# Kernel optimization log

Hardware: AMD Instinct MI355X
Metric: run time of the kernel (lower is better)

The kernel has to match this reference:

```python
import jax, jax.numpy as jnp
import numpy as np

B, H, S, D = 2, 16, 2048, 64

def setup_inputs() -> dict:
    key = jax.random.key(0)
    kq, kk, kv, km = jax.random.split(key, 4)
    Q = jax.random.normal(kq, (B, H, S, D), dtype=jnp.float32)
    K = jax.random.normal(kk, (B, H, S, D), dtype=jnp.float32)
    V = jax.random.normal(kv, (B, H, S, D), dtype=jnp.float32)
    # padding-style boolean mask, broadcast over heads; True = masked out
    attn_mask = jax.random.randint(km, (B, 1, S, S), 0, 2).astype(jnp.bool_)
    return {"Q": Q, "K": K, "V": V, "attn_mask": attn_mask}

def reference(Q, K, V, attn_mask):
    d = Q.shape[-1]
    scale = 1.0 / np.sqrt(d).astype(np.float32)
    # [B,H,S,S] scores
    scores = jnp.einsum('bhqd,bhkd->bhqk', Q, K) * scale
    scores = jnp.where(attn_mask, jnp.float32(-1e9), scores)
    attn = jax.nn.softmax(scores, axis=-1)
    context = jnp.einsum('bhqk,bhkd->bhqd', attn, V)
    return context
```

## Files before the change

### kernel.cpp

```cpp
#include <hip/hip_runtime.h>

#define B_ 2
#define H_ 16
#define S_ 2048
#define D_ 64
#define BK 32
#define NKT (S_ / BK)
#define QSCALE 0.18033688011112042f
#define MFIX 16.0f

#define KSD 36
#define VTD 18
#define KS_SZ (BK * KSD)
#define VT_SZ (D_ * VTD)

typedef __attribute__((ext_vector_type(4))) float  float4v;
typedef __attribute__((ext_vector_type(2))) _Float16 half2v;
typedef __attribute__((ext_vector_type(4))) _Float16 half4v;
typedef __attribute__((ext_vector_type(8))) _Float16 half8v;
typedef __attribute__((ext_vector_type(2))) __fp16 fp16x2;
typedef __attribute__((ext_vector_type(2))) unsigned uint2v;

union H2U { half2v h; fp16x2 g; unsigned u; };
union H4U { half4v h4; half2v h2[2]; fp16x2 g2[2]; uint2v u2; };
union H8U { half8v h8; fp16x2 g2[4]; };

__device__ __forceinline__ unsigned pkh(float a, float b) {
    H2U c; c.g = __builtin_amdgcn_cvt_pkrtz(a, b);
    return c.u;
}
__device__ __forceinline__ float fexp2(float x) {
#if __has_builtin(__builtin_amdgcn_exp2f)
    return __builtin_amdgcn_exp2f(x);
#else
    return exp2f(x);
#endif
}

__device__ __forceinline__ void wg_barrier() {
    asm volatile("s_waitcnt lgkmcnt(0)\n\ts_barrier" ::: "memory");
}

struct Stage { float4 k0, k1, va, vb; };

__device__ __forceinline__ void stage_load(const float* __restrict__ Kg,
                                           const float* __restrict__ Vg,
                                           int kk, int dd, Stage& s) {
    s.k0 = *(const float4*)(Kg + (size_t)kk * D_ + dd);
    s.k1 = *(const float4*)(Kg + (size_t)(kk + 16) * D_ + dd);
    s.va = *(const float4*)(Vg + (size_t)(2 * kk) * D_ + dd);
    s.vb = *(const float4*)(Vg + (size_t)(2 * kk + 1) * D_ + dd);
}

__device__ __forceinline__ void stage_store(unsigned* KsB, unsigned* VtB,
                                            int kwa, int kwb, const int* vw,
                                            const Stage& s) {
    *(uint2v*)&KsB[kwa] = (uint2v){ pkh(s.k0.x, s.k0.y), pkh(s.k0.z, s.k0.w) };
    *(uint2v*)&KsB[kwb] = (uint2v){ pkh(s.k1.x, s.k1.y), pkh(s.k1.z, s.k1.w) };
    VtB[vw[0]] = pkh(s.va.x, s.vb.x);
    VtB[vw[1]] = pkh(s.va.y, s.vb.y);
    VtB[vw[2]] = pkh(s.va.z, s.vb.z);
    VtB[vw[3]] = pkh(s.va.w, s.vb.w);
}

__device__ __forceinline__ float4 mask2bias(int4 m) {
    float4 r;
    r.x = m.x ? -1e9f : -MFIX;  r.y = m.y ? -1e9f : -MFIX;
    r.z = m.z ? -1e9f : -MFIX;  r.w = m.w ? -1e9f : -MFIX;
    return r;
}

__global__ __launch_bounds__(256, 4)
void attn_flash_st(const float* __restrict__ Q, const float* __restrict__ K,
                   const float* __restrict__ V, const int* __restrict__ mask,
                   float* __restrict__ out)
{
    __shared__ unsigned KsAll[2 * KS_SZ];
    __shared__ unsigned VtAll[2 * VT_SZ];

    const int tid  = threadIdx.x;
    const int lane = tid & 63;
    const int l15  = lane & 15;
    const int quad = lane >> 4;
    const int wave = tid >> 6;
    const int bh   = blockIdx.y;
    const int b    = bh / H_;
    const int qbase = blockIdx.x * 64 + wave * 16;
    const size_t qkv = (size_t)bh * S_ * D_;

    half8v qf[2];
    {
        const float* qrow = Q + qkv + (size_t)(qbase + l15) * D_ + quad * 8;
        #pragma unroll
        for (int dc = 0; dc < 2; ++dc) {
            float4 f0 = *(const float4*)(qrow + dc * 32);
            float4 f1 = *(const float4*)(qrow + dc * 32 + 4);
            H8U u;
            u.g2[0] = __builtin_amdgcn_cvt_pkrtz(f0.x * QSCALE, f0.y * QSCALE);
            u.g2[1] = __builtin_amdgcn_cvt_pkrtz(f0.z * QSCALE, f0.w * QSCALE);
            u.g2[2] = __builtin_amdgcn_cvt_pkrtz(f1.x * QSCALE, f1.y * QSCALE);
            u.g2[3] = __builtin_amdgcn_cvt_pkrtz(f1.z * QSCALE, f1.w * QSCALE);
            qf[dc] = u.h8;
        }
    }

    const int kk = tid >> 4;
    const int dd = (tid & 15) * 4;
    const int kwa = kk * KSD + (tid & 15) * 2;
    const int kwb = (kk + 16) * KSD + (tid & 15) * 2;
    int vw[4];
    #pragma unroll
    for (int m = 0; m < 4; ++m)
        vw[m] = (dd + m) * VTD + (kk ^ ((((dd + m) >> 4) & 3) << 1));

    int kroff[2][2];
    #pragma unroll
    for (int t = 0; t < 2; ++t)
        #pragma unroll
        for (int dc = 0; dc < 2; ++dc)
            kroff[t][dc] = (t * 16 + l15) * KSD + dc * 16 + quad * 4;
    int vrd[4][2];
    #pragma unroll
    for (int nb = 0; nb < 4; ++nb)
        #pragma unroll
        for (int t = 0; t < 2; ++t)
            vrd[nb][t] = (nb * 16 + l15) * VTD + ((t * 8 + quad * 2) ^ ((nb & 3) << 1));

    const int* mrow0 = mask + (size_t)b * S_ * S_ + (size_t)(qbase + l15) * S_ + quad * 4;

    float l_lane = 0.0f;
    float4v o[4];
    #pragma unroll
    for (int nb = 0; nb < 4; ++nb) o[nb] = (float4v){0.f, 0.f, 0.f, 0.f};

    const float* Kg0 = K + qkv;
    const float* Vg0 = V + qkv;

    Stage sA, sB;
    stage_load(Kg0, Vg0, kk, dd, sA);
    stage_store(KsAll, VtAll, kwa, kwb, vw, sA);
    stage_load(Kg0 + BK * D_, Vg0 + BK * D_, kk, dd, sB);
    float4 mk0 = mask2bias(*(const int4*)(mrow0));
    float4 mk1 = mask2bias(*(const int4*)(mrow0 + 16));
    wg_barrier();

    auto iter = [&](int kt, const unsigned* KsB, const unsigned* VtB,
                    unsigned* KsN, unsigned* VtN, Stage& pre, Stage& sto) {
        const int ktn = (kt + 2 < NKT) ? kt + 2 : NKT - 1;
        stage_load(Kg0 + (size_t)ktn * BK * D_, Vg0 + (size_t)ktn * BK * D_, kk, dd, pre);
        const int mtn = (kt + 1 < NKT) ? kt + 1 : NKT - 1;
        const int* mnext = mrow0 + (size_t)mtn * BK;
        const float4 nm0 = mask2bias(*(const int4*)(mnext));
        const float4 nm1 = mask2bias(*(const int4*)(mnext + 16));

        float4v st0 = (float4v){0.f,0.f,0.f,0.f}, st1 = st0;
        {
            half8v kf;
            kf = *(const half8v*)&KsB[kroff[0][0]];
            st0 = __builtin_amdgcn_mfma_f32_16x16x32_f16(kf, qf[0], st0, 0, 0, 0);
            kf = *(const half8v*)&KsB[kroff[0][1]];
            st0 = __builtin_amdgcn_mfma_f32_16x16x32_f16(kf, qf[1], st0, 0, 0, 0);
            kf = *(const half8v*)&KsB[kroff[1][0]];
            st1 = __builtin_amdgcn_mfma_f32_16x16x32_f16(kf, qf[0], st1, 0, 0, 0);
            kf = *(const half8v*)&KsB[kroff[1][1]];
            st1 = __builtin_amdgcn_mfma_f32_16x16x32_f16(kf, qf[1], st1, 0, 0, 0);
        }

        float4v p0, p1;
        p0.x = fexp2(st0.x + mk0.x); p0.y = fexp2(st0.y + mk0.y);
        p0.z = fexp2(st0.z + mk0.z); p0.w = fexp2(st0.w + mk0.w);
        p1.x = fexp2(st1.x + mk1.x); p1.y = fexp2(st1.y + mk1.y);
        p1.z = fexp2(st1.z + mk1.z); p1.w = fexp2(st1.w + mk1.w);

        l_lane += ((p0.x + p0.y) + (p0.z + p0.w)) +
                  ((p1.x + p1.y) + (p1.z + p1.w));

        H4U pf0u, pf1u;
        pf0u.g2[0] = __builtin_amdgcn_cvt_pkrtz(p0.x, p0.y);
        pf0u.g2[1] = __builtin_amdgcn_cvt_pkrtz(p0.z, p0.w);
        pf1u.g2[0] = __builtin_amdgcn_cvt_pkrtz(p1.x, p1.y);
        pf1u.g2[1] = __builtin_amdgcn_cvt_pkrtz(p1.z, p1.w);

        #pragma unroll
        for (int nb = 0; nb < 4; ++nb) {
            H4U vf;
            vf.u2 = *(const uint2v*)&VtB[vrd[nb][0]];
            o[nb] = __builtin_amdgcn_mfma_f32_16x16x16f16(vf.h4, pf0u.h4, o[nb], 0, 0, 0);
            vf.u2 = *(const uint2v*)&VtB[vrd[nb][1]];
            o[nb] = __builtin_amdgcn_mfma_f32_16x16x16f16(vf.h4, pf1u.h4, o[nb], 0, 0, 0);
        }

        stage_store(KsN, VtN, kwa, kwb, vw, sto);
        wg_barrier();
        mk0 = nm0; mk1 = nm1;
    };

    #pragma unroll 1
    for (int kt2 = 0; kt2 < NKT; kt2 += 2) {
        iter(kt2,     KsAll,         VtAll,         (unsigned*)KsAll + KS_SZ, (unsigned*)VtAll + VT_SZ, sA, sB);
        iter(kt2 + 1, KsAll + KS_SZ, VtAll + VT_SZ, (unsigned*)KsAll,         (unsigned*)VtAll,         sB, sA);
    }

    float ls = l_lane;
    ls += __shfl_xor(ls, 16, 64);
    ls += __shfl_xor(ls, 32, 64);
    const float inv = 1.0f / ls;

    float* orow = out + qkv + (size_t)(qbase + l15) * D_ + quad * 4;
    #pragma unroll
    for (int nb = 0; nb < 4; ++nb) {
        float4 ov = { o[nb].x * inv, o[nb].y * inv, o[nb].z * inv, o[nb].w * inv };
        *(float4*)(orow + nb * 16) = ov;
    }
}

extern "C" void kernel_launch(void* const* d_in, const int* in_sizes, int n_in,
                              void* d_out, int out_size, void* d_ws, size_t ws_size,
                              hipStream_t stream) {
    const float* Q    = (const float*)d_in[0];
    const float* K    = (const float*)d_in[1];
    const float* V    = (const float*)d_in[2];
    const int*   mask = (const int*)d_in[3];
    float* out = (float*)d_out;

    dim3 grid(S_ / 64, B_ * H_);
    dim3 block(256);
    attn_flash_st<<<grid, block, 0, stream>>>(Q, K, V, mask, out);
}
```

Measured before the change: 196.7 us.

## Split key dimension across two blocks and combine partial outputs

Adds a split-K flash attention path: each of two z-blocks handles half the key tiles and writes unnormalized partial outputs and row sums to workspace, then a combine kernel sums and normalizes them. This doubles the grid to raise parallelism and occupancy (launch bounds raised to 8 blocks) on a grid of only 1024 blocks. It costs extra global traffic for the partials and a second kernel launch, and it falls back to the old kernel if the workspace is too small. The fixed softmax offset makes the partials directly additive without max rescaling.

```diff
diff --git a/kernel.cpp b/kernel.cpp
--- a/kernel.cpp
+++ b/kernel.cpp
@@ -6,6 +6,8 @@
 #define D_ 64
 #define BK 32
 #define NKT (S_ / BK)
+#define ZSPLIT 2
+#define NKT_Z (NKT / ZSPLIT)
 #define QSCALE 0.18033688011112042f
 #define MFIX 16.0f
 
@@ -13,6 +15,9 @@
 #define VTD 18
 #define KS_SZ (BK * KSD)
 #define VT_SZ (D_ * VTD)
+
+#define BHSD ((size_t)B_ * H_ * S_ * D_)
+#define BHS  ((size_t)B_ * H_ * S_)
 
 typedef __attribute__((ext_vector_type(4))) float  float4v;
 typedef __attribute__((ext_vector_type(2))) _Float16 half2v;
@@ -70,10 +75,10 @@
     return r;
 }
 
-__global__ __launch_bounds__(256, 4)
-void attn_flash_st(const float* __restrict__ Q, const float* __restrict__ K,
+__global__ __launch_bounds__(256, 8)
+void attn_flash_sk(const float* __restrict__ Q, const float* __restrict__ K,
                    const float* __restrict__ V, const int* __restrict__ mask,
-                   float* __restrict__ out)
+                   float* __restrict__ Opart, float* __restrict__ Lpart)
 {
     __shared__ unsigned KsAll[2 * KS_SZ];
     __shared__ unsigned VtAll[2 * VT_SZ];
@@ -88,6 +93,9 @@
     const int qbase = blockIdx.x * 64 + wave * 16;
     const size_t qkv = (size_t)bh * S_ * D_;
 
+    const int ktBegin = blockIdx.z * NKT_Z;
+    const int ktEnd   = ktBegin + NKT_Z;
+
     half8v qf[2];
     {
         const float* qrow = Q + qkv + (size_t)(qbase + l15) * D_ + quad * 8;
@@ -137,18 +145,18 @@
     const float* Vg0 = V + qkv;
 
     Stage sA, sB;
-    stage_load(Kg0, Vg0, kk, dd, sA);
+    stage_load(Kg0 + (size_t)ktBegin * BK * D_, Vg0 + (size_t)ktBegin * BK * D_, kk, dd, sA);
     stage_store(KsAll, VtAll, kwa, kwb, vw, sA);
-    stage_load(Kg0 + BK * D_, Vg0 + BK * D_, kk, dd, sB);
-    float4 mk0 = mask2bias(*(const int4*)(mrow0));
-    float4 mk1 = mask2bias(*(const int4*)(mrow0 + 16));
+    stage_load(Kg0 + (size_t)(ktBegin + 1) * BK * D_, Vg0 + (size_t)(ktBegin + 1) * BK * D_, kk, dd, sB);
+    float4 mk0 = mask2bias(*(const int4*)(mrow0 + (size_t)ktBegin * BK));
+    float4 mk1 = mask2bias(*(const int4*)(mrow0 + (size_t)ktBegin * BK + 16));
     wg_barrier();
 
     auto iter = [&](int kt, const unsigned* KsB, const unsigned* VtB,
                     unsigned* KsN, unsigned* VtN, Stage& pre, Stage& sto) {
-        const int ktn = (kt + 2 < NKT) ? kt + 2 : NKT - 1;
+        const int ktn = (kt + 2 < ktEnd) ? kt + 2 : ktEnd - 1;
         stage_load(Kg0 + (size_t)ktn * BK * D_, Vg0 + (size_t)ktn * BK * D_, kk, dd, pre);
-        const int mtn = (kt + 1 < NKT) ? kt + 1 : NKT - 1;
+        const int mtn = (kt + 1 < ktEnd) ? kt + 1 : ktEnd - 1;
         const int* mnext = mrow0 + (size_t)mtn * BK;
         const float4 nm0 = mask2bias(*(const int4*)(mnext));
         const float4 nm1 = mask2bias(*(const int4*)(mnext + 16));
@@ -196,6 +204,167 @@
     };
 
     #pragma unroll 1
+    for (int kt2 = ktBegin; kt2 < ktEnd; kt2 += 2) {
+        iter(kt2,     KsAll,         VtAll,         (unsigned*)KsAll + KS_SZ, (unsigned*)VtAll + VT_SZ, sA, sB);
+        iter(kt2 + 1, KsAll + KS_SZ, VtAll + VT_SZ, (unsigned*)KsAll,         (unsigned*)VtAll,         sB, sA);
+    }
+
+    float ls = l_lane;
+    ls += __shfl_xor(ls, 16, 64);
+    ls += __shfl_xor(ls, 32, 64);
+
+    float* orow = Opart + (size_t)blockIdx.z * BHSD + qkv
+                  + (size_t)(qbase + l15) * D_ + quad * 4;
+    #pragma unroll
+    for (int nb = 0; nb < 4; ++nb) {
+        float4 ov = { o[nb].x, o[nb].y, o[nb].z, o[nb].w };
+        *(float4*)(orow + nb * 16) = ov;
+    }
+    if (quad == 0)
+        Lpart[(size_t)blockIdx.z * BHS + (size_t)bh * S_ + qbase + l15] = ls;
+}
+
+__global__ __launch_bounds__(256)
+void attn_combine(const float* __restrict__ Opart, const float* __restrict__ Lpart,
+                  float* __restrict__ out)
+{
+    const size_t i = (size_t)blockIdx.x * 256 + threadIdx.x;
+    const size_t row = i >> 4;
+    const float l = Lpart[row] + Lpart[BHS + row];
+    const float inv = 1.0f / l;
+    const float4 a = ((const float4*)Opart)[i];
+    const float4 c = ((const float4*)Opart)[BHSD / 4 + i];
+    float4 r = { (a.x + c.x) * inv, (a.y + c.y) * inv,
+                 (a.z + c.z) * inv, (a.w + c.w) * inv };
+    ((float4*)out)[i] = r;
+}
+
+__global__ __launch_bounds__(256, 4)
+void attn_flash_st(const float* __restrict__ Q, const float* __restrict__ K,
+                   const float* __restrict__ V, const int* __restrict__ mask,
+                   float* __restrict__ out)
+{
+    __shared__ unsigned KsAll[2 * KS_SZ];
+    __shared__ unsigned VtAll[2 * VT_SZ];
+
+    const int tid  = threadIdx.x;
+    const int lane = tid & 63;
+    const int l15  = lane & 15;
+    const int quad = lane >> 4;
+    const int wave = tid >> 6;
+    const int bh   = blockIdx.y;
+    const int b    = bh / H_;
+    const int qbase = blockIdx.x * 64 + wave * 16;
+    const size_t qkv = (size_t)bh * S_ * D_;
+
+    half8v qf[2];
+    {
+        const float* qrow = Q + qkv + (size_t)(qbase + l15) * D_ + quad * 8;
+        #pragma unroll
+        for (int dc = 0; dc < 2; ++dc) {
+            float4 f0 = *(const float4*)(qrow + dc * 32);
+            float4 f1 = *(const float4*)(qrow + dc * 32 + 4);
+            H8U u;
+            u.g2[0] = __builtin_amdgcn_cvt_pkrtz(f0.x * QSCALE, f0.y * QSCALE);
+            u.g2[1] = __builtin_amdgcn_cvt_pkrtz(f0.z * QSCALE, f0.w * QSCALE);
+            u.g2[2] = __builtin_amdgcn_cvt_pkrtz(f1.x * QSCALE, f1.y * QSCALE);
+            u.g2[3] = __builtin_amdgcn_cvt_pkrtz(f1.z * QSCALE, f1.w * QSCALE);
+            qf[dc] = u.h8;
+        }
+    }
+
+    const int kk = tid >> 4;
+    const int dd = (tid & 15) * 4;
+    const int kwa = kk * KSD + (tid & 15) * 2;
+    const int kwb = (kk + 16) * KSD + (tid & 15) * 2;
+    int vw[4];
+    #pragma unroll
+    for (int m = 0; m < 4; ++m)
+        vw[m] = (dd + m) * VTD + (kk ^ ((((dd + m) >> 4) & 3) << 1));
+
+    int kroff[2][2];
+    #pragma unroll
+    for (int t = 0; t < 2; ++t)
+        #pragma unroll
+        for (int dc = 0; dc < 2; ++dc)
+            kroff[t][dc] = (t * 16 + l15) * KSD + dc * 16 + quad * 4;
+    int vrd[4][2];
+    #pragma unroll
+    for (int nb = 0; nb < 4; ++nb)
+        #pragma unroll
+        for (int t = 0; t < 2; ++t)
+            vrd[nb][t] = (nb * 16 + l15) * VTD + ((t * 8 + quad * 2) ^ ((nb & 3) << 1));
+
+    const int* mrow0 = mask + (size_t)b * S_ * S_ + (size_t)(qbase + l15) * S_ + quad * 4;
+
+    float l_lane = 0.0f;
+    float4v o[4];
+    #pragma unroll
+    for (int nb = 0; nb < 4; ++nb) o[nb] = (float4v){0.f, 0.f, 0.f, 0.f};
+
+    const float* Kg0 = K + qkv;
+    const float* Vg0 = V + qkv;
+
+    Stage sA, sB;
+    stage_load(Kg0, Vg0, kk, dd, sA);
+    stage_store(KsAll, VtAll, kwa, kwb, vw, sA);
+    stage_load(Kg0 + BK * D_, Vg0 + BK * D_, kk, dd, sB);
+    float4 mk0 = mask2bias(*(const int4*)(mrow0));
+    float4 mk1 = mask2bias(*(const int4*)(mrow0 + 16));
+    wg_barrier();
+
+    auto iter = [&](int kt, const unsigned* KsB, const unsigned* VtB,
+                    unsigned* KsN, unsigned* VtN, Stage& pre, Stage& sto) {
+        const int ktn = (kt + 2 < NKT) ? kt + 2 : NKT - 1;
+        stage_load(Kg0 + (size_t)ktn * BK * D_, Vg0 + (size_t)ktn * BK * D_, kk, dd, pre);
+        const int mtn = (kt + 1 < NKT) ? kt + 1 : NKT - 1;
+        const int* mnext = mrow0 + (size_t)mtn * BK;
+        const float4 nm0 = mask2bias(*(const int4*)(mnext));
+        const float4 nm1 = mask2bias(*(const int4*)(mnext + 16));
+
+        float4v st0 = (float4v){0.f,0.f,0.f,0.f}, st1 = st0;
+        {
+            half8v kf;
+            kf = *(const half8v*)&KsB[kroff[0][0]];
+            st0 = __builtin_amdgcn_mfma_f32_16x16x32_f16(kf, qf[0], st0, 0, 0, 0);
+            kf = *(const half8v*)&KsB[kroff[0][1]];
+            st0 = __builtin_amdgcn_mfma_f32_16x16x32_f16(kf, qf[1], st0, 0, 0, 0);
+            kf = *(const half8v*)&KsB[kroff[1][0]];
+            st1 = __builtin_amdgcn_mfma_f32_16x16x32_f16(kf, qf[0], st1, 0, 0, 0);
+            kf = *(const half8v*)&KsB[kroff[1][1]];
+            st1 = __builtin_amdgcn_mfma_f32_16x16x32_f16(kf, qf[1], st1, 0, 0, 0);
+        }
+
+        float4v p0, p1;
+        p0.x = fexp2(st0.x + mk0.x); p0.y = fexp2(st0.y + mk0.y);
+        p0.z = fexp2(st0.z + mk0.z); p0.w = fexp2(st0.w + mk0.w);
+        p1.x = fexp2(st1.x + mk1.x); p1.y = fexp2(st1.y + mk1.y);
+        p1.z = fexp2(st1.z + mk1.z); p1.w = fexp2(st1.w + mk1.w);
+
+        l_lane += ((p0.x + p0.y) + (p0.z + p0.w)) +
+                  ((p1.x + p1.y) + (p1.z + p1.w));
+
+        H4U pf0u, pf1u;
+        pf0u.g2[0] = __builtin_amdgcn_cvt_pkrtz(p0.x, p0.y);
+        pf0u.g2[1] = __builtin_amdgcn_cvt_pkrtz(p0.z, p0.w);
+        pf1u.g2[0] = __builtin_amdgcn_cvt_pkrtz(p1.x, p1.y);
+        pf1u.g2[1] = __builtin_amdgcn_cvt_pkrtz(p1.z, p1.w);
+
+        #pragma unroll
+        for (int nb = 0; nb < 4; ++nb) {
+            H4U vf;
+            vf.u2 = *(const uint2v*)&VtB[vrd[nb][0]];
+            o[nb] = __builtin_amdgcn_mfma_f32_16x16x16f16(vf.h4, pf0u.h4, o[nb], 0, 0, 0);
+            vf.u2 = *(const uint2v*)&VtB[vrd[nb][1]];
+            o[nb] = __builtin_amdgcn_mfma_f32_16x16x16f16(vf.h4, pf1u.h4, o[nb], 0, 0, 0);
+        }
+
+        stage_store(KsN, VtN, kwa, kwb, vw, sto);
+        wg_barrier();
+        mk0 = nm0; mk1 = nm1;
+    };
+
+    #pragma unroll 1
     for (int kt2 = 0; kt2 < NKT; kt2 += 2) {
         iter(kt2,     KsAll,         VtAll,         (unsigned*)KsAll + KS_SZ, (unsigned*)VtAll + VT_SZ, sA, sB);
         iter(kt2 + 1, KsAll + KS_SZ, VtAll + VT_SZ, (unsigned*)KsAll,         (unsigned*)VtAll,         sB, sA);
@@ -223,7 +392,19 @@
     const int*   mask = (const int*)d_in[3];
     float* out = (float*)d_out;
 
-    dim3 grid(S_ / 64, B_ * H_);
-    dim3 block(256);
-    attn_flash_st<<<grid, block, 0, stream>>>(Q, K, V, mask, out);
-}
+    const size_t opBytes = BHSD * ZSPLIT * sizeof(float);
+    const size_t lpBytes = BHS  * ZSPLIT * sizeof(float);
+    const size_t needFull = opBytes + lpBytes;
+
+    if (d_ws && ws_size >= needFull) {
+        float* Opart = (float*)d_ws;
+        float* Lpart = (float*)((char*)d_ws + opBytes);
+        attn_flash_sk<<<dim3(S_ / 64, B_ * H_, ZSPLIT), dim3(256), 0, stream>>>(
+            Q, K, V, mask, Opart, Lpart);
+        attn_combine<<<dim3((unsigned)(BHSD / 4 / 256)), dim3(256), 0, stream>>>(
+            Opart, Lpart, out);
+    } else {
+        attn_flash_st<<<dim3(S_ / 64, B_ * H_), dim3(256), 0, stream>>>(
+            Q, K, V, mask, out);
+    }
+}
```

Measured after the change: 601.4 us. 3.06x slower.

## Software-pipeline softmax of tile k with PV matmul of tile k-1

Applied to the files above, without the earlier changes.

Restructures the key-tile loop so each iteration issues the QK^T MFMAs for the current tile, then the PV MFMAs for the previous tile's probabilities, then computes exp/convert for the current tile. The goal is to hide the exp and convert latency behind independent MFMA work and break the serial QK→softmax→PV dependency chain. The V tile is now triple-buffered in LDS, with a prologue, a loop unrolled by six and an epilogue. This adds shared memory and register pressure and makes the buffer rotation more intricate.

```diff
diff --git a/kernel.cpp b/kernel.cpp
--- a/kernel.cpp
+++ b/kernel.cpp
@@ -71,12 +71,12 @@
 }
 
 __global__ __launch_bounds__(256, 4)
-void attn_flash_st(const float* __restrict__ Q, const float* __restrict__ K,
+void attn_flash_pl(const float* __restrict__ Q, const float* __restrict__ K,
                    const float* __restrict__ V, const int* __restrict__ mask,
                    float* __restrict__ out)
 {
-    __shared__ unsigned KsAll[2 * KS_SZ];
-    __shared__ unsigned VtAll[2 * VT_SZ];
+    __shared__ unsigned Ks[2 * KS_SZ];
+    __shared__ unsigned Vt[3 * VT_SZ];
 
     const int tid  = threadIdx.x;
     const int lane = tid & 63;
@@ -132,20 +132,56 @@
     float4v o[4];
     #pragma unroll
     for (int nb = 0; nb < 4; ++nb) o[nb] = (float4v){0.f, 0.f, 0.f, 0.f};
+    H4U pfP0, pfP1;
 
     const float* Kg0 = K + qkv;
     const float* Vg0 = V + qkv;
 
     Stage sA, sB;
     stage_load(Kg0, Vg0, kk, dd, sA);
-    stage_store(KsAll, VtAll, kwa, kwb, vw, sA);
+    stage_store(Ks, Vt, kwa, kwb, vw, sA);
     stage_load(Kg0 + BK * D_, Vg0 + BK * D_, kk, dd, sB);
     float4 mk0 = mask2bias(*(const int4*)(mrow0));
     float4 mk1 = mask2bias(*(const int4*)(mrow0 + 16));
     wg_barrier();
 
-    auto iter = [&](int kt, const unsigned* KsB, const unsigned* VtB,
-                    unsigned* KsN, unsigned* VtN, Stage& pre, Stage& sto) {
+    auto qkmm = [&](const unsigned* KsC, float4v& st0, float4v& st1) {
+        half8v kf;
+        kf = *(const half8v*)&KsC[kroff[0][0]];
+        st0 = __builtin_amdgcn_mfma_f32_16x16x32_f16(kf, qf[0], st0, 0, 0, 0);
+        kf = *(const half8v*)&KsC[kroff[0][1]];
+        st0 = __builtin_amdgcn_mfma_f32_16x16x32_f16(kf, qf[1], st0, 0, 0, 0);
+        kf = *(const half8v*)&KsC[kroff[1][0]];
+        st1 = __builtin_amdgcn_mfma_f32_16x16x32_f16(kf, qf[0], st1, 0, 0, 0);
+        kf = *(const half8v*)&KsC[kroff[1][1]];
+        st1 = __builtin_amdgcn_mfma_f32_16x16x32_f16(kf, qf[1], st1, 0, 0, 0);
+    };
+    auto softmax_cvt = [&](const float4v& st0, const float4v& st1) {
+        float4v p0, p1;
+        p0.x = fexp2(st0.x + mk0.x); p0.y = fexp2(st0.y + mk0.y);
+        p0.z = fexp2(st0.z + mk0.z); p0.w = fexp2(st0.w + mk0.w);
+        p1.x = fexp2(st1.x + mk1.x); p1.y = fexp2(st1.y + mk1.y);
+        p1.z = fexp2(st1.z + mk1.z); p1.w = fexp2(st1.w + mk1.w);
+        l_lane += ((p0.x + p0.y) + (p0.z + p0.w)) +
+                  ((p1.x + p1.y) + (p1.z + p1.w));
+        pfP0.g2[0] = __builtin_amdgcn_cvt_pkrtz(p0.x, p0.y);
+        pfP0.g2[1] = __builtin_amdgcn_cvt_pkrtz(p0.z, p0.w);
+        pfP1.g2[0] = __builtin_amdgcn_cvt_pkrtz(p1.x, p1.y);
+        pfP1.g2[1] = __builtin_amdgcn_cvt_pkrtz(p1.z, p1.w);
+    };
+    auto pvmm = [&](const unsigned* VtP) {
+        #pragma unroll
+        for (int nb = 0; nb < 4; ++nb) {
+            H4U vf;
+            vf.u2 = *(const uint2v*)&VtP[vrd[nb][0]];
+            o[nb] = __builtin_amdgcn_mfma_f32_16x16x16f16(vf.h4, pfP0.h4, o[nb], 0, 0, 0);
+            vf.u2 = *(const uint2v*)&VtP[vrd[nb][1]];
+            o[nb] = __builtin_amdgcn_mfma_f32_16x16x16f16(vf.h4, pfP1.h4, o[nb], 0, 0, 0);
+        }
+    };
+
+    auto iterD = [&](int kt, const unsigned* KsC, const unsigned* VtP,
+                     unsigned* KsN, unsigned* VtN, Stage& pre, Stage& sto) {
         const int ktn = (kt + 2 < NKT) ? kt + 2 : NKT - 1;
         stage_load(Kg0 + (size_t)ktn * BK * D_, Vg0 + (size_t)ktn * BK * D_, kk, dd, pre);
         const int mtn = (kt + 1 < NKT) ? kt + 1 : NKT - 1;
@@ -154,52 +190,41 @@
         const float4 nm1 = mask2bias(*(const int4*)(mnext + 16));
 
         float4v st0 = (float4v){0.f,0.f,0.f,0.f}, st1 = st0;
-        {
-            half8v kf;
-            kf = *(const half8v*)&KsB[kroff[0][0]];
-            st0 = __builtin_amdgcn_mfma_f32_16x16x32_f16(kf, qf[0], st0, 0, 0, 0);
-            kf = *(const half8v*)&KsB[kroff[0][1]];
-            st0 = __builtin_amdgcn_mfma_f32_16x16x32_f16(kf, qf[1], st0, 0, 0, 0);
-            kf = *(const half8v*)&KsB[kroff[1][0]];
-            st1 = __builtin_amdgcn_mfma_f32_16x16x32_f16(kf, qf[0], st1, 0, 0, 0);
-            kf = *(const half8v*)&KsB[kroff[1][1]];
-            st1 = __builtin_amdgcn_mfma_f32_16x16x32_f16(kf, qf[1], st1, 0, 0, 0);
-        }
-
-        float4v p0, p1;
-        p0.x = fexp2(st0.x + mk0.x); p0.y = fexp2(st0.y + mk0.y);
-        p0.z = fexp2(st0.z + mk0.z); p0.w = fexp2(st0.w + mk0.w);
-        p1.x = fexp2(st1.x + mk1.x); p1.y = fexp2(st1.y + mk1.y);
-        p1.z = fexp2(st1.z + mk1.z); p1.w = fexp2(st1.w + mk1.w);
-
-        l_lane += ((p0.x + p0.y) + (p0.z + p0.w)) +
-                  ((p1.x + p1.y) + (p1.z + p1.w));
-
-        H4U pf0u, pf1u;
-        pf0u.g2[0] = __builtin_amdgcn_cvt_pkrtz(p0.x, p0.y);
-        pf0u.g2[1] = __builtin_amdgcn_cvt_pkrtz(p0.z, p0.w);
-        pf1u.g2[0] = __builtin_amdgcn_cvt_pkrtz(p1.x, p1.y);
-        pf1u.g2[1] = __builtin_amdgcn_cvt_pkrtz(p1.z, p1.w);
-
-        #pragma unroll
-        for (int nb = 0; nb < 4; ++nb) {
-            H4U vf;
-            vf.u2 = *(const uint2v*)&VtB[vrd[nb][0]];
-            o[nb] = __builtin_amdgcn_mfma_f32_16x16x16f16(vf.h4, pf0u.h4, o[nb], 0, 0, 0);
-            vf.u2 = *(const uint2v*)&VtB[vrd[nb][1]];
-            o[nb] = __builtin_amdgcn_mfma_f32_16x16x16f16(vf.h4, pf1u.h4, o[nb], 0, 0, 0);
-        }
-
+        qkmm(KsC, st0, st1);
+        pvmm(VtP);
         stage_store(KsN, VtN, kwa, kwb, vw, sto);
+        softmax_cvt(st0, st1);
         wg_barrier();
         mk0 = nm0; mk1 = nm1;
     };
 
+    {
+        stage_load(Kg0 + 2 * BK * D_, Vg0 + 2 * BK * D_, kk, dd, sA);
+        const int* mnext = mrow0 + BK;
+        const float4 nm0 = mask2bias(*(const int4*)(mnext));
+        const float4 nm1 = mask2bias(*(const int4*)(mnext + 16));
+        float4v st0 = (float4v){0.f,0.f,0.f,0.f}, st1 = st0;
+        qkmm(Ks, st0, st1);
+        stage_store(Ks + KS_SZ, Vt + VT_SZ, kwa, kwb, vw, sB);
+        softmax_cvt(st0, st1);
+        wg_barrier();
+        mk0 = nm0; mk1 = nm1;
+    }
+
     #pragma unroll 1
-    for (int kt2 = 0; kt2 < NKT; kt2 += 2) {
-        iter(kt2,     KsAll,         VtAll,         (unsigned*)KsAll + KS_SZ, (unsigned*)VtAll + VT_SZ, sA, sB);
-        iter(kt2 + 1, KsAll + KS_SZ, VtAll + VT_SZ, (unsigned*)KsAll,         (unsigned*)VtAll,         sB, sA);
-    }
+    for (int t = 0; t < 10; ++t) {
+        const int k = 1 + 6 * t;
+        iterD(k,     Ks + KS_SZ, Vt,             Ks,         Vt + 2*VT_SZ, sB, sA);
+        iterD(k + 1, Ks,         Vt + VT_SZ,     Ks + KS_SZ, Vt,           sA, sB);
+        iterD(k + 2, Ks + KS_SZ, Vt + 2*VT_SZ,   Ks,         Vt + VT_SZ,   sB, sA);
+        iterD(k + 3, Ks,         Vt,             Ks + KS_SZ, Vt + 2*VT_SZ, sA, sB);
+        iterD(k + 4, Ks + KS_SZ, Vt + VT_SZ,     Ks,         Vt,           sB, sA);
+        iterD(k + 5, Ks,         Vt + 2*VT_SZ,   Ks + KS_SZ, Vt + VT_SZ,   sA, sB);
+    }
+    iterD(61, Ks + KS_SZ, Vt,             Ks,         Vt + 2*VT_SZ, sB, sA);
+    iterD(62, Ks,         Vt + VT_SZ,     Ks + KS_SZ, Vt,           sA, sB);
+    iterD(63, Ks + KS_SZ, Vt + 2*VT_SZ,   Ks,         Vt + VT_SZ,   sB, sA);
+    pvmm(Vt);
 
     float ls = l_lane;
     ls += __shfl_xor(ls, 16, 64);
@@ -223,7 +248,6 @@
     const int*   mask = (const int*)d_in[3];
     float* out = (float*)d_out;
 
-    dim3 grid(S_ / 64, B_ * H_);
-    dim3 block(256);
-    attn_flash_st<<<grid, block, 0, stream>>>(Q, K, V, mask, out);
-}
+    attn_flash_pl<<<dim3(S_ / 64, B_ * H_), dim3(256), 0, stream>>>(
+        Q, K, V, mask, out);
+}
```

New measurement: 215.7 us. 1.1x slower.

## Pre-pack K/V into MFMA fragment layout and split KV across blocks

Applied to the files above, without the earlier changes.

Adds a pre-pass kernel that converts K and V to fp16 and stores them in a global image already arranged in per-lane MFMA fragment order. The main kernel then loads fragments straight from global memory with no LDS staging or barriers, and splits the KV range in two (split-K) with an XCD-aware block mapping. A combine kernel adds the two partial outputs and divides by the summed denominators. This removes LDS traffic and synchronisation and doubles the block count, at the cost of two extra launches, fp32 partial buffers in workspace, and an extra pass over the output. The old kernel remains as a fallback when the workspace is too small.

```diff
diff --git a/kernel.cpp b/kernel.cpp
--- a/kernel.cpp
+++ b/kernel.cpp
@@ -9,10 +9,13 @@
 #define QSCALE 0.18033688011112042f
 #define MFIX 16.0f
 
-#define KSD 36
-#define VTD 18
-#define KS_SZ (BK * KSD)
-#define VT_SZ (D_ * VTD)
+#define KFRAG_OFF(t, dc) (((t) * 2 + (dc)) * 256)
+#define VFRAG_OFF(nb, t) (1024 + ((nb) * 2 + (t)) * 128)
+#define TILE2_DW 2048
+
+#define BHSD ((size_t)B_ * H_ * S_ * D_)
+#define BHS  ((size_t)B_ * H_ * S_)
+#define IMG2_DW ((size_t)B_ * H_ * NKT * TILE2_DW)
 
 typedef __attribute__((ext_vector_type(4))) float  float4v;
 typedef __attribute__((ext_vector_type(2))) _Float16 half2v;
@@ -20,10 +23,11 @@
 typedef __attribute__((ext_vector_type(8))) _Float16 half8v;
 typedef __attribute__((ext_vector_type(2))) __fp16 fp16x2;
 typedef __attribute__((ext_vector_type(2))) unsigned uint2v;
+typedef __attribute__((ext_vector_type(4))) unsigned uint4v;
 
 union H2U { half2v h; fp16x2 g; unsigned u; };
 union H4U { half4v h4; half2v h2[2]; fp16x2 g2[2]; uint2v u2; };
-union H8U { half8v h8; fp16x2 g2[4]; };
+union H8U { half8v h8; fp16x2 g2[4]; uint4v u4; };
 
 __device__ __forceinline__ unsigned pkh(float a, float b) {
     H2U c; c.g = __builtin_amdgcn_cvt_pkrtz(a, b);
@@ -39,6 +43,192 @@
 
 __device__ __forceinline__ void wg_barrier() {
     asm volatile("s_waitcnt lgkmcnt(0)\n\ts_barrier" ::: "memory");
+}
+
+__global__ __launch_bounds__(256)
+void pack_kv2(const float* __restrict__ K, const float* __restrict__ V,
+              unsigned* __restrict__ img)
+{
+    __shared__ float Kf[32 * 64];
+    __shared__ float Vf[32 * 64];
+    const int tid = threadIdx.x;
+    const int kt = blockIdx.x, bh = blockIdx.y;
+    const size_t base = ((size_t)bh * S_ + (size_t)kt * 32) * D_;
+
+    const int rr = tid >> 4, c4 = (tid & 15) * 4;
+    *(float4*)&Kf[rr * 64 + c4]        = *(const float4*)(K + base + (size_t)rr * D_ + c4);
+    *(float4*)&Kf[(rr + 16) * 64 + c4] = *(const float4*)(K + base + (size_t)(rr + 16) * D_ + c4);
+    *(float4*)&Vf[rr * 64 + c4]        = *(const float4*)(V + base + (size_t)rr * D_ + c4);
+    *(float4*)&Vf[(rr + 16) * 64 + c4] = *(const float4*)(V + base + (size_t)(rr + 16) * D_ + c4);
+    __syncthreads();
+
+    unsigned* out = img + (size_t)(bh * NKT + kt) * TILE2_DW;
+    const int lane = tid & 63, wave = tid >> 6;
+    const int l15 = lane & 15, quad = lane >> 4;
+
+    if (wave < 2) {
+        const int t = wave;
+        const int row = t * 16 + l15;
+        #pragma unroll
+        for (int dc = 0; dc < 2; ++dc) {
+            const int d0 = dc * 32 + quad * 8;
+            const float* kr = &Kf[row * 64 + d0];
+            uint4v v = { pkh(kr[0], kr[1]), pkh(kr[2], kr[3]),
+                         pkh(kr[4], kr[5]), pkh(kr[6], kr[7]) };
+            *(uint4v*)&out[KFRAG_OFF(t, dc) + lane * 4] = v;
+        }
+    } else {
+        const int nbb = (wave - 2) * 2;
+        #pragma unroll
+        for (int nbo = 0; nbo < 2; ++nbo) {
+            const int nb = nbb + nbo;
+            const int d = nb * 16 + l15;
+            #pragma unroll
+            for (int t = 0; t < 2; ++t) {
+                const int k0 = t * 16 + quad * 4;
+                uint2v v = { pkh(Vf[k0 * 64 + d],       Vf[(k0 + 1) * 64 + d]),
+                             pkh(Vf[(k0 + 2) * 64 + d], Vf[(k0 + 3) * 64 + d]) };
+                *(uint2v*)&out[VFRAG_OFF(nb, t) + lane * 2] = v;
+            }
+        }
+    }
+}
+
+__global__ __launch_bounds__(256, 4)
+void attn_frag(const float* __restrict__ Q, const unsigned* __restrict__ img,
+               const int* __restrict__ mask,
+               float* __restrict__ Opart, float* __restrict__ Lpart)
+{
+    const int tid  = threadIdx.x;
+    const int lane = tid & 63;
+    const int l15  = lane & 15;
+    const int quad = lane >> 4;
+    const int wave = tid >> 6;
+
+    const int id    = blockIdx.x;
+    const int xcd   = id & 7;
+    const int local = id >> 3;
+    const int bh_l  = local >> 6;
+    const int rem   = local & 63;
+    const int z     = rem >> 5;
+    const int qb    = rem & 31;
+    const int bh    = xcd * 4 + bh_l;
+    const int b     = bh / H_;
+    const int qbase = qb * 64 + wave * 16;
+    const size_t qkv = (size_t)bh * S_ * D_;
+    const int ktB = z * (NKT / 2);
+
+    half8v qf[2];
+    {
+        const float* qrow = Q + qkv + (size_t)(qbase + l15) * D_ + quad * 8;
+        #pragma unroll
+        for (int dc = 0; dc < 2; ++dc) {
+            float4 f0 = *(const float4*)(qrow + dc * 32);
+            float4 f1 = *(const float4*)(qrow + dc * 32 + 4);
+            H8U u;
+            u.g2[0] = __builtin_amdgcn_cvt_pkrtz(f0.x * QSCALE, f0.y * QSCALE);
+            u.g2[1] = __builtin_amdgcn_cvt_pkrtz(f0.z * QSCALE, f0.w * QSCALE);
+            u.g2[2] = __builtin_amdgcn_cvt_pkrtz(f1.x * QSCALE, f1.y * QSCALE);
+            u.g2[3] = __builtin_amdgcn_cvt_pkrtz(f1.z * QSCALE, f1.w * QSCALE);
+            qf[dc] = u.h8;
+        }
+    }
+
+    const unsigned* tp  = img + (size_t)(bh * NKT + ktB) * TILE2_DW;
+    const unsigned* kfb = tp + lane * 4;
+    const unsigned* vfb = tp + lane * 2;
+
+    const int* mrow = mask + (size_t)b * S_ * S_ + (size_t)(qbase + l15) * S_
+                      + quad * 4 + (size_t)ktB * BK;
+
+    float l_lane = 0.0f;
+    float4v o[4];
+    #pragma unroll
+    for (int nb = 0; nb < 4; ++nb) o[nb] = (float4v){0.f, 0.f, 0.f, 0.f};
+
+    #pragma unroll 2
+    for (int ktl = 0; ktl < NKT / 2; ++ktl) {
+        H8U k00, k01, k10, k11;
+        k00.u4 = *(const uint4v*)(kfb + KFRAG_OFF(0, 0));
+        k01.u4 = *(const uint4v*)(kfb + KFRAG_OFF(0, 1));
+        k10.u4 = *(const uint4v*)(kfb + KFRAG_OFF(1, 0));
+        k11.u4 = *(const uint4v*)(kfb + KFRAG_OFF(1, 1));
+        H4U v00, v01, v10, v11, v20, v21, v30, v31;
+        v00.u2 = *(const uint2v*)(vfb + VFRAG_OFF(0, 0));
+        v01.u2 = *(const uint2v*)(vfb + VFRAG_OFF(0, 1));
+        v10.u2 = *(const uint2v*)(vfb + VFRAG_OFF(1, 0));
+        v11.u2 = *(const uint2v*)(vfb + VFRAG_OFF(1, 1));
+        v20.u2 = *(const uint2v*)(vfb + VFRAG_OFF(2, 0));
+        v21.u2 = *(const uint2v*)(vfb + VFRAG_OFF(2, 1));
+        v30.u2 = *(const uint2v*)(vfb + VFRAG_OFF(3, 0));
+        v31.u2 = *(const uint2v*)(vfb + VFRAG_OFF(3, 1));
+        const int4 m0 = *(const int4*)(mrow);
+        const int4 m1 = *(const int4*)(mrow + 16);
+        kfb += TILE2_DW; vfb += TILE2_DW; mrow += BK;
+
+        float4v st0 = (float4v){0.f, 0.f, 0.f, 0.f}, st1 = st0;
+        st0 = __builtin_amdgcn_mfma_f32_16x16x32_f16(k00.h8, qf[0], st0, 0, 0, 0);
+        st0 = __builtin_amdgcn_mfma_f32_16x16x32_f16(k01.h8, qf[1], st0, 0, 0, 0);
+        st1 = __builtin_amdgcn_mfma_f32_16x16x32_f16(k10.h8, qf[0], st1, 0, 0, 0);
+        st1 = __builtin_amdgcn_mfma_f32_16x16x32_f16(k11.h8, qf[1], st1, 0, 0, 0);
+
+        float4v p0, p1;
+        p0.x = fexp2(st0.x + (m0.x ? -1e9f : -MFIX));
+        p0.y = fexp2(st0.y + (m0.y ? -1e9f : -MFIX));
+        p0.z = fexp2(st0.z + (m0.z ? -1e9f : -MFIX));
+        p0.w = fexp2(st0.w + (m0.w ? -1e9f : -MFIX));
+        p1.x = fexp2(st1.x + (m1.x ? -1e9f : -MFIX));
+        p1.y = fexp2(st1.y + (m1.y ? -1e9f : -MFIX));
+        p1.z = fexp2(st1.z + (m1.z ? -1e9f : -MFIX));
+        p1.w = fexp2(st1.w + (m1.w ? -1e9f : -MFIX));
+
+        l_lane += ((p0.x + p0.y) + (p0.z + p0.w)) +
+                  ((p1.x + p1.y) + (p1.z + p1.w));
+
+        H4U pf0, pf1;
+        pf0.g2[0] = __builtin_amdgcn_cvt_pkrtz(p0.x, p0.y);
+        pf0.g2[1] = __builtin_amdgcn_cvt_pkrtz(p0.z, p0.w);
+        pf1.g2[0] = __builtin_amdgcn_cvt_pkrtz(p1.x, p1.y);
+        pf1.g2[1] = __builtin_amdgcn_cvt_pkrtz(p1.z, p1.w);
+
+        o[0] = __builtin_amdgcn_mfma_f32_16x16x16f16(v00.h4, pf0.h4, o[0], 0, 0, 0);
+        o[0] = __builtin_amdgcn_mfma_f32_16x16x16f16(v01.h4, pf1.h4, o[0], 0, 0, 0);
+        o[1] = __builtin_amdgcn_mfma_f32_16x16x16f16(v10.h4, pf0.h4, o[1], 0, 0, 0);
+        o[1] = __builtin_amdgcn_mfma_f32_16x16x16f16(v11.h4, pf1.h4, o[1], 0, 0, 0);
+        o[2] = __builtin_amdgcn_mfma_f32_16x16x16f16(v20.h4, pf0.h4, o[2], 0, 0, 0);
+        o[2] = __builtin_amdgcn_mfma_f32_16x16x16f16(v21.h4, pf1.h4, o[2], 0, 0, 0);
+        o[3] = __builtin_amdgcn_mfma_f32_16x16x16f16(v30.h4, pf0.h4, o[3], 0, 0, 0);
+        o[3] = __builtin_amdgcn_mfma_f32_16x16x16f16(v31.h4, pf1.h4, o[3], 0, 0, 0);
+    }
+
+    float ls = l_lane;
+    ls += __shfl_xor(ls, 16, 64);
+    ls += __shfl_xor(ls, 32, 64);
+
+    float* orow = Opart + (size_t)z * BHSD + qkv
+                  + (size_t)(qbase + l15) * D_ + quad * 4;
+    #pragma unroll
+    for (int nb = 0; nb < 4; ++nb) {
+        float4 ov = { o[nb].x, o[nb].y, o[nb].z, o[nb].w };
+        *(float4*)(orow + nb * 16) = ov;
+    }
+    if (quad == 0)
+        Lpart[(size_t)z * BHS + (size_t)bh * S_ + qbase + l15] = ls;
+}
+
+__global__ __launch_bounds__(256)
+void attn_combine(const float* __restrict__ Opart, const float* __restrict__ Lpart,
+                  float* __restrict__ out)
+{
+    const size_t i = (size_t)blockIdx.x * 256 + threadIdx.x;
+    const size_t row = i >> 4;
+    const float l = Lpart[row] + Lpart[BHS + row];
+    const float inv = 1.0f / l;
+    const float4 a = ((const float4*)Opart)[i];
+    const float4 c = ((const float4*)Opart)[BHSD / 4 + i];
+    float4 r = { (a.x + c.x) * inv, (a.y + c.y) * inv,
+                 (a.z + c.z) * inv, (a.w + c.w) * inv };
+    ((float4*)out)[i] = r;
 }
 
 struct Stage { float4 k0, k1, va, vb; };
@@ -51,6 +241,11 @@
     s.va = *(const float4*)(Vg + (size_t)(2 * kk) * D_ + dd);
     s.vb = *(const float4*)(Vg + (size_t)(2 * kk + 1) * D_ + dd);
 }
+
+#define KSD 36
+#define VTD 18
+#define KS_SZ (BK * KSD)
+#define VT_SZ (D_ * VTD)
 
 __device__ __forceinline__ void stage_store(unsigned* KsB, unsigned* VtB,
                                             int kwa, int kwb, const int* vw,
@@ -223,7 +418,20 @@
     const int*   mask = (const int*)d_in[3];
     float* out = (float*)d_out;
 
-    dim3 grid(S_ / 64, B_ * H_);
-    dim3 block(256);
-    attn_flash_st<<<grid, block, 0, stream>>>(Q, K, V, mask, out);
-}
+    const size_t imgBytes = IMG2_DW * sizeof(unsigned);
+    const size_t opBytes  = BHSD * 2 * sizeof(float);
+    const size_t lpBytes  = BHS  * 2 * sizeof(float);
+
+    if (d_ws && ws_size >= imgBytes + opBytes + lpBytes) {
+        unsigned* img = (unsigned*)d_ws;
+        float* Opart = (float*)((char*)d_ws + imgBytes);
+        float* Lpart = (float*)((char*)d_ws + imgBytes + opBytes);
+        pack_kv2<<<dim3(NKT, B_ * H_), dim3(256), 0, stream>>>(K, V, img);
+        attn_frag<<<dim3(2048), dim3(256), 0, stream>>>(Q, img, mask, Opart, Lpart);
+        attn_combine<<<dim3((unsigned)(BHSD / 4 / 256)), dim3(256), 0, stream>>>(
+            Opart, Lpart, out);
+    } else {
+        attn_flash_st<<<dim3(S_ / 64, B_ * H_), dim3(256), 0, stream>>>(
+            Q, K, V, mask, out);
+    }
+}
```

Result: slower. 276.1 us (+40.3%).
